# Performance work log

Hardware: AMD Instinct MI355X
Metric: run time of the kernel (lower is better)

## Reference

```python
import jax, jax.numpy as jnp
import numpy as np

DROPOUT_RATE = 0.5
CONF_THRESH = 0.85
IGNORE_VALUE = 2
EPS = 1e-07


def setup_inputs() -> dict:
    key = jax.random.key(0)
    k1, k2 = jax.random.split(key)
    B, H, W = 16, 1024, 1024
    pred = jax.random.uniform(k1, (B, H, W), dtype=jnp.float32)
    mask = jax.random.randint(k2, (B, H, W), 0, 3, dtype=jnp.int32)
    return {"pred": pred, "mask": mask}


def _training_need_score(pred, gt, confidence):
    # Higher = needs more training: CW=4, UW=3, UC=2, CC=1 (+/- confidence bonus)
    is_correct = (pred > 0.5) == (gt == 1.0)
    is_conf = confidence > CONF_THRESH
    score = jnp.where(is_conf & is_correct, 1.0,
            jnp.where(~is_conf & is_correct, 2.0,
            jnp.where(~is_conf & ~is_correct, 3.0, 4.0))).astype(pred.dtype)
    bonus = (confidence - 0.5) * 0.5
    return jnp.where(is_correct, score - bonus, score + bonus)


def _dynamic_masks(pred, mask):
    # Vectorized equivalent of the per-batch nonzero/argsort/scatter loop:
    # rank annotated pixels per batch by descending need-score; top n_train -> train.
    B, H, W = mask.shape
    annotated = (mask != IGNORE_VALUE).reshape(B, H * W)
    gt = mask.astype(pred.dtype)
    confidence = jnp.maximum(pred, 1.0 - pred)
    scores = _training_need_score(pred, gt, confidence).reshape(B, H * W)
    neg_inf = jnp.asarray(-jnp.inf, scores.dtype)
    masked_scores = jnp.where(annotated, scores, neg_inf)
    order = jnp.argsort(-masked_scores, axis=1)          # descending score order
    rank = jnp.argsort(order, axis=1)                    # rank of each pixel in that order
    n_points = annotated.sum(axis=1)
    n_train = (n_points.astype(jnp.float32) * (1.0 - DROPOUT_RATE)).astype(jnp.int32)
    train = annotated & (rank < n_train[:, None])
    holdout = annotated & ~train
    return train.reshape(B, H, W), holdout.reshape(B, H, W)


def reference(pred, mask):
    if pred.ndim == 4 and pred.shape[1] == 1:
        pred = pred[:, 0]
    train_mask, holdout_mask = _dynamic_masks(pred, mask)
    gt = mask.astype(pred.dtype)
    p = jnp.clip(pred, EPS, 1.0 - EPS)
    bce = -(gt * jnp.log(p) + (1.0 - gt) * jnp.log(1.0 - p))
    tm = train_mask.astype(pred.dtype)
    loss = (bce * tm).sum() / (tm.sum() + EPS)
    return loss, train_mask, holdout_mask
```

## Files before the change

### kernel.cpp

```cpp
#include <hip/hip_runtime.h>
#include <stdint.h>

#define NBATCH 16
#define HW_ (1 << 20)
#define TPB 256

#define NBPB_H 32
#define TPB_H 512
#define EPB_H (HW_ / NBPB_H)
#define ITER_H (EPB_H / (TPB_H * 4))

#define NBINS 8192
#define FBASE 0x3F400

#define NBPB_F 256
#define FCHUNK (HW_ / NBPB_F)

#define CAND_CAP 32768
#define LCAP 512
#define TIE_CAP 4096
#define CNT_STRIDE 64

typedef float f4v __attribute__((ext_vector_type(4)));

struct BParams {
    unsigned int k;
    unsigned int bin1f;
    unsigned int r;
    unsigned int mode;
};

__device__ __forceinline__ unsigned int score_bits(float p, int m) {
    bool correct = (p > 0.5f) == (m == 1);
    float conf = fmaxf(p, 1.0f - p);
    float base = correct ? ((conf > 0.85f) ? 1.0f : 2.0f)
                         : ((conf > 0.85f) ? 4.0f : 3.0f);
    float bonus = (conf - 0.5f) * 0.5f;
    float s = correct ? (base - bonus) : (base + bonus);
    return __float_as_uint(s);
}

__global__ void k_hist(const float4* __restrict__ pred4, const int4* __restrict__ mask4,
                       unsigned int* __restrict__ slices) {
    __shared__ unsigned int lh[NBINS];
    int b = blockIdx.x / NBPB_H;
    int blk = blockIdx.x % NBPB_H;
    for (int i = threadIdx.x; i < NBINS; i += TPB_H) lh[i] = 0;
    __syncthreads();
    int l4base = blk * (EPB_H / 4);
    for (int j = 0; j < ITER_H; j++) {
        int i4l = l4base + j * TPB_H + threadIdx.x;
        size_t g4 = (size_t)b * (HW_ / 4) + i4l;
        float4 p = pred4[g4];
        int4 m = mask4[g4];
        float pa[4] = {p.x, p.y, p.z, p.w};
        int ma[4] = {m.x, m.y, m.z, m.w};
#pragma unroll
        for (int l = 0; l < 4; l++) {
            if (ma[l] != 2) {
                unsigned int sb = score_bits(pa[l], ma[l]);
                int fb = (int)(sb >> 12) - FBASE;
                fb = min(max(fb, 0), NBINS - 1);
                atomicAdd(&lh[fb], 1u);
            }
        }
    }
    __syncthreads();
    unsigned int* sp = slices + (size_t)blockIdx.x * NBINS;
    for (int i = threadIdx.x; i < NBINS; i += TPB_H)
        sp[i] = lh[i];
}

__global__ void k_find(const unsigned int* __restrict__ slices, BParams* __restrict__ prm,
                       unsigned int* __restrict__ cand_cnt) {
    int bb = blockIdx.x;
    int t = threadIdx.x;
    __shared__ unsigned int hist[NBINS];
    __shared__ unsigned int cs_[257];
    unsigned int acc[32];
#pragma unroll
    for (int j = 0; j < 32; j++) acc[j] = 0;
    const unsigned int* base = slices + (size_t)bb * NBPB_H * NBINS;
    for (int s = 0; s < NBPB_H; s++) {
        const unsigned int* sp = base + (size_t)s * NBINS;
#pragma unroll
        for (int j = 0; j < 32; j++) acc[j] += sp[j * 256 + t];
    }
#pragma unroll
    for (int j = 0; j < 32; j++) hist[j * 256 + t] = acc[j];
    if (t == 0) cand_cnt[bb * CNT_STRIDE] = 0;
    __syncthreads();
    {
        unsigned int gs = 0;
#pragma unroll
        for (int j = 0; j < 32; j++) gs += hist[t * 32 + j];
        cs_[t] = gs;
        if (t == 0) cs_[256] = 0;
    }
    __syncthreads();
    for (int off = 1; off < 256; off <<= 1) {
        unsigned int a = (t + off < 256) ? cs_[t + off] : 0u;
        __syncthreads();
        cs_[t] += a;
        __syncthreads();
    }
    unsigned int n = cs_[0];
    unsigned int k = (unsigned int)(int)((float)n * 0.5f);
    if (k == 0) {
        if (t == 0) {
            BParams P; P.k = 0; P.bin1f = 0xFFFFFFFFu; P.r = 0; P.mode = 0;
            prm[bb] = P;
        }
        return;
    }
    if (cs_[t] >= k && cs_[t + 1] < k) {
        unsigned int cum = cs_[t + 1];
        for (int j = 31; j >= 0; j--) {
            unsigned int hb = hist[t * 32 + j];
            if (cum + hb >= k) {
                BParams P;
                P.k = k;
                P.bin1f = (unsigned int)(FBASE + t * 32 + j);
                P.r = k - cum;
                P.mode = 1;
                prm[bb] = P;
                break;
            }
            cum += hb;
        }
    }
}

__global__ void k_main(const float4* __restrict__ pred4, const int4* __restrict__ mask4,
                       const BParams* __restrict__ prm, float* __restrict__ out,
                       float* __restrict__ partials, unsigned int* __restrict__ cand_cnt,
                       unsigned int* __restrict__ cand_idx, unsigned int* __restrict__ cand_sb,
                       float* __restrict__ cand_bce) {
    int b = blockIdx.x / NBPB_F;
    int blk = blockIdx.x % NBPB_F;
    BParams P = prm[b];
    unsigned int target = P.bin1f;
    __shared__ unsigned int lcode[FCHUNK / 4];
    __shared__ float red[TPB];
    __shared__ unsigned int l_idx[LCAP];
    __shared__ unsigned int l_sb[LCAP];
    __shared__ float l_bce[LCAP];
    __shared__ unsigned int lcnt;
    __shared__ unsigned int gbase;
    if (threadIdx.x == 0) lcnt = 0;
    __syncthreads();
    float acc = 0.0f;
    int ibase = blk * FCHUNK;
    for (int j = 0; j < FCHUNK / (TPB * 4); j++) {
        int v = j * TPB + threadIdx.x;
        size_t g4 = (size_t)b * (HW_ / 4) + (ibase / 4) + v;
        float4 p = pred4[g4];
        int4 m = mask4[g4];
        float pa[4] = {p.x, p.y, p.z, p.w};
        int ma[4] = {m.x, m.y, m.z, m.w};
        unsigned int cw = 0;
#pragma unroll
        for (int l = 0; l < 4; l++) {
            bool ann = (ma[l] != 2);
            unsigned int sb = score_bits(pa[l], ma[l]);
            unsigned int fine = sb >> 12;
            bool tr = ann && (fine > target);
            bool amb = ann && (fine == target);
            unsigned int code = (tr ? 1u : 0u) | ((ann && !tr) ? 2u : 0u);
            cw |= code << (8 * l);
            float bce = 0.0f;
            if (tr || amb) {
                float pc = fminf(fmaxf(pa[l], 1e-7f), 1.0f - 1e-7f);
                bce = (ma[l] == 1) ? -__logf(pc) : -__logf(1.0f - pc);
            }
            if (tr) acc += bce;
            if (amb) {
                unsigned int p0 = atomicAdd(&lcnt, 1u);
                if (p0 < LCAP) {
                    l_idx[p0] = (unsigned int)(ibase + v * 4 + l);
                    l_sb[p0] = sb;
                    l_bce[p0] = bce;
                } else {
                    unsigned int gp = atomicAdd(&cand_cnt[b * CNT_STRIDE], 1u);
                    if (gp < CAND_CAP) {
                        size_t o = (size_t)b * CAND_CAP + gp;
                        cand_idx[o] = (unsigned int)(ibase + v * 4 + l);
                        cand_sb[o] = sb;
                        cand_bce[o] = bce;
                    }
                }
            }
        }
        lcode[v] = cw;
    }
    __syncthreads();
    unsigned int n = min(lcnt, (unsigned int)LCAP);
    if (threadIdx.x == 0 && n > 0)
        gbase = atomicAdd(&cand_cnt[b * CNT_STRIDE], n);
    __syncthreads();
    for (unsigned int i = threadIdx.x; i < n; i += TPB) {
        unsigned int pos = gbase + i;
        if (pos < CAND_CAP) {
            size_t o = (size_t)b * CAND_CAP + pos;
            cand_idx[o] = l_idx[i];
            cand_sb[o] = l_sb[i];
            cand_bce[o] = l_bce[i];
        }
    }
    float* trout = out + 1;
    float* hoout = out + 1 + (size_t)NBATCH * HW_;
    size_t Gbase = (size_t)b * HW_ + (size_t)ibase;
    for (int v = threadIdx.x; v < FCHUNK / 4 - 1; v += TPB) {
        unsigned int w0 = lcode[v];
        unsigned int w1 = lcode[v + 1];
        unsigned int c0 = (w0 >> 24) & 0xFFu;
        unsigned int c1 = w1 & 0xFFu;
        unsigned int c2 = (w1 >> 8) & 0xFFu;
        unsigned int c3 = (w1 >> 16) & 0xFFu;
        int e = 3 + 4 * v;
        f4v tv = { (float)(c0 & 1u), (float)(c1 & 1u), (float)(c2 & 1u), (float)(c3 & 1u) };
        f4v hv = { (float)((c0 >> 1) & 1u), (float)((c1 >> 1) & 1u),
                   (float)((c2 >> 1) & 1u), (float)((c3 >> 1) & 1u) };
        __builtin_nontemporal_store(tv, (f4v*)(trout + Gbase + e));
        __builtin_nontemporal_store(hv, (f4v*)(hoout + Gbase + e));
    }
    if (threadIdx.x < 3) {
        unsigned int c = (lcode[0] >> (8 * threadIdx.x)) & 0xFFu;
        trout[Gbase + threadIdx.x] = (float)(c & 1u);
        hoout[Gbase + threadIdx.x] = (float)((c >> 1) & 1u);
    }
    if (threadIdx.x == 3) {
        unsigned int c = (lcode[FCHUNK / 4 - 1] >> 24) & 0xFFu;
        trout[Gbase + FCHUNK - 1] = (float)(c & 1u);
        hoout[Gbase + FCHUNK - 1] = (float)((c >> 1) & 1u);
    }
    red[threadIdx.x] = acc;
    __syncthreads();
    for (int off = TPB / 2; off > 0; off >>= 1) {
        if (threadIdx.x < off) red[threadIdx.x] += red[threadIdx.x + off];
        __syncthreads();
    }
    if (threadIdx.x == 0) partials[blockIdx.x] = red[0];
}

__global__ void k_fixup(const unsigned int* __restrict__ cand_cnt,
                        const unsigned int* __restrict__ cand_idx,
                        const unsigned int* __restrict__ cand_sb,
                        const float* __restrict__ cand_bce,
                        const BParams* __restrict__ prm, float* __restrict__ out,
                        float* __restrict__ tie_partials) {
    int b = blockIdx.x;
    int t = threadIdx.x;
    __shared__ unsigned int h[4096];
    __shared__ unsigned int cs_[257];
    __shared__ unsigned int tie_idx[TIE_CAP];
    __shared__ unsigned int misc[8];
    __shared__ float red[TPB];
    BParams P = prm[b];
    if (P.mode == 0) {
        if (t == 0) tie_partials[b] = 0.0f;
        return;
    }
    unsigned int C = cand_cnt[b * CNT_STRIDE];
    if (C > CAND_CAP) C = CAND_CAP;
    const unsigned int* ci = cand_idx + (size_t)b * CAND_CAP;
    const unsigned int* cs = cand_sb + (size_t)b * CAND_CAP;
    const float* cb = cand_bce + (size_t)b * CAND_CAP;
    for (int i = t; i < 4096; i += TPB) h[i] = 0;
    if (t < 8) misc[t] = (t == 4) ? 0xFFFFFFFFu : 0u;
    __syncthreads();
    for (unsigned int i = t; i < C; i += TPB)
        atomicAdd(&h[cs[i] & 0xFFFu], 1u);
    __syncthreads();
    {
        unsigned int gs = 0;
#pragma unroll
        for (int j = 0; j < 16; j++) gs += h[t * 16 + j];
        cs_[t] = gs;
        if (t == 0) cs_[256] = 0;
    }
    __syncthreads();
    for (int off = 1; off < 256; off <<= 1) {
        unsigned int a = (t + off < 256) ? cs_[t + off] : 0u;
        __syncthreads();
        cs_[t] += a;
        __syncthreads();
    }
    if (cs_[t] >= P.r && cs_[t + 1] < P.r) {
        unsigned int cum = cs_[t + 1];
        for (int j = 15; j >= 0; j--) {
            unsigned int hb = h[t * 16 + j];
            if (cum + hb >= P.r) {
                unsigned int T = P.r - cum;
                misc[0] = (unsigned int)(t * 16 + j);
                misc[1] = T;
                misc[2] = (T == hb) ? 1u : 0u;
                break;
            }
            cum += hb;
        }
    }
    __syncthreads();
    unsigned int vstar = misc[0], T = misc[1];
    bool allTies = (misc[2] != 0);
    unsigned int idxcut;
    if (allTies) {
        idxcut = 0xFFFFFFFFu;
    } else {
        for (unsigned int i = t; i < C; i += TPB) {
            if ((cs[i] & 0xFFFu) == vstar) {
                unsigned int p = atomicAdd(&misc[3], 1u);
                if (p < TIE_CAP) tie_idx[p] = ci[i];
            }
        }
        __syncthreads();
        unsigned int E2 = misc[3];
        if (E2 > TIE_CAP) E2 = TIE_CAP;
        for (unsigned int i = t; i < E2; i += TPB) {
            unsigned int vi = tie_idx[i];
            unsigned int cnt = 0;
            for (unsigned int j = 0; j < E2; j++) cnt += (tie_idx[j] < vi) ? 1u : 0u;
            if (cnt == T - 1) misc[4] = vi;
        }
        __syncthreads();
        idxcut = misc[4];
    }
    float acc = 0.0f;
    float* trout = out + 1;
    float* hoout = out + 1 + (size_t)NBATCH * HW_;
    size_t base = (size_t)b * HW_;
    for (unsigned int i = t; i < C; i += TPB) {
        unsigned int low = cs[i] & 0xFFFu;
        bool tr = (low > vstar) || (low == vstar && ci[i] <= idxcut);
        if (tr) {
            trout[base + ci[i]] = 1.0f;
            hoout[base + ci[i]] = 0.0f;
            acc += cb[i];
        }
    }
    red[t] = acc;
    __syncthreads();
    for (int off = TPB / 2; off > 0; off >>= 1) {
        if (t < off) red[t] += red[t + off];
        __syncthreads();
    }
    if (t == 0) tie_partials[b] = red[0];
}

__global__ void k_loss(const float* __restrict__ partials, const float* __restrict__ tie_partials,
                       const BParams* __restrict__ prm, float* __restrict__ out) {
    __shared__ double red[TPB];
    double s = 0.0;
    for (int i = threadIdx.x; i < NBATCH * NBPB_F; i += TPB) s += (double)partials[i];
    if (threadIdx.x < NBATCH) s += (double)tie_partials[threadIdx.x];
    red[threadIdx.x] = s;
    __syncthreads();
    for (int off = TPB / 2; off > 0; off >>= 1) {
        if (threadIdx.x < off) red[threadIdx.x] += red[threadIdx.x + off];
        __syncthreads();
    }
    if (threadIdx.x == 0) {
        unsigned long long den = 0;
        for (int b = 0; b < NBATCH; b++) den += prm[b].k;
        float denf = (float)den + 1e-7f;
        out[0] = (float)red[0] / denf;
    }
}

extern "C" void kernel_launch(void* const* d_in, const int* in_sizes, int n_in,
                              void* d_out, int out_size, void* d_ws, size_t ws_size,
                              hipStream_t stream) {
    const float4* pred4 = (const float4*)d_in[0];
    const int4* mask4 = (const int4*)d_in[1];
    float* out = (float*)d_out;

    unsigned int* slices = (unsigned int*)d_ws;
    unsigned int* cand_cnt = slices + (size_t)NBATCH * NBPB_H * NBINS;
    BParams* prm = (BParams*)(cand_cnt + NBATCH * CNT_STRIDE);
    float* partials = (float*)(prm + NBATCH);
    float* tie_partials = partials + NBATCH * NBPB_F;
    unsigned int* cand_idx = (unsigned int*)(tie_partials + NBATCH);
    unsigned int* cand_sb = cand_idx + NBATCH * CAND_CAP;
    float* cand_bce = (float*)(cand_sb + NBATCH * CAND_CAP);

    k_hist<<<dim3(NBATCH * NBPB_H), dim3(TPB_H), 0, stream>>>(pred4, mask4, slices);
    k_find<<<dim3(NBATCH), dim3(TPB), 0, stream>>>(slices, prm, cand_cnt);
    k_main<<<dim3(NBATCH * NBPB_F), dim3(TPB), 0, stream>>>(pred4, mask4, prm, out, partials,
                                                            cand_cnt, cand_idx, cand_sb, cand_bce);
    k_fixup<<<dim3(NBATCH), dim3(TPB), 0, stream>>>(cand_cnt, cand_idx, cand_sb, cand_bce,
                                                    prm, out, tie_partials);
    k_loss<<<dim3(1), dim3(TPB), 0, stream>>>(partials, tie_partials, prm, out);
}
```

Measured before the change: 302.0 us.

## Fuse five kernels into two using last-block-done atomic counters

Folds the histogram-merge and threshold search into the last histogram block of each batch, and folds the tie fixup and final loss reduction into the last main block of each batch and overall. Per-block atomic done-counters with threadfences replace kernel boundaries, and block sums go into double atomics instead of a partials array. A memset now resets the counters before each launch. The aim is to remove launch gaps and the serial single-block kernels, at the cost of the tail work running inside one late block. TIE_CAP is also reduced so the shared-memory union fits.

```diff
diff --git a/kernel.cpp b/kernel.cpp
--- a/kernel.cpp
+++ b/kernel.cpp
@@ -18,8 +18,8 @@
 
 #define CAND_CAP 32768
 #define LCAP 512
-#define TIE_CAP 4096
-#define CNT_STRIDE 64
+#define TIE_CAP 1024
+#define CSTR 64
 
 typedef float f4v __attribute__((ext_vector_type(4)));
 
@@ -40,16 +40,20 @@
     return __float_as_uint(s);
 }
 
-__global__ void k_hist(const float4* __restrict__ pred4, const int4* __restrict__ mask4,
-                       unsigned int* __restrict__ slices) {
+__global__ void k_histfind(const float4* __restrict__ pred4, const int4* __restrict__ mask4,
+                           unsigned int* __restrict__ slices, unsigned int* __restrict__ doneA,
+                           BParams* __restrict__ prm) {
     __shared__ unsigned int lh[NBINS];
+    __shared__ unsigned int cs_[TPB_H + 1];
+    __shared__ unsigned int lastFlag;
     int b = blockIdx.x / NBPB_H;
     int blk = blockIdx.x % NBPB_H;
-    for (int i = threadIdx.x; i < NBINS; i += TPB_H) lh[i] = 0;
+    int t = threadIdx.x;
+    for (int i = t; i < NBINS; i += TPB_H) lh[i] = 0;
     __syncthreads();
     int l4base = blk * (EPB_H / 4);
     for (int j = 0; j < ITER_H; j++) {
-        int i4l = l4base + j * TPB_H + threadIdx.x;
+        int i4l = l4base + j * TPB_H + t;
         size_t g4 = (size_t)b * (HW_ / 4) + i4l;
         float4 p = pred4[g4];
         int4 m = mask4[g4];
@@ -67,39 +71,38 @@
     }
     __syncthreads();
     unsigned int* sp = slices + (size_t)blockIdx.x * NBINS;
-    for (int i = threadIdx.x; i < NBINS; i += TPB_H)
-        sp[i] = lh[i];
-}
-
-__global__ void k_find(const unsigned int* __restrict__ slices, BParams* __restrict__ prm,
-                       unsigned int* __restrict__ cand_cnt) {
-    int bb = blockIdx.x;
-    int t = threadIdx.x;
-    __shared__ unsigned int hist[NBINS];
-    __shared__ unsigned int cs_[257];
-    unsigned int acc[32];
-#pragma unroll
-    for (int j = 0; j < 32; j++) acc[j] = 0;
-    const unsigned int* base = slices + (size_t)bb * NBPB_H * NBINS;
+    for (int i = t; i < NBINS; i += TPB_H) sp[i] = lh[i];
+    __syncthreads();
+    if (t == 0) {
+        __threadfence();
+        unsigned int old = atomicAdd(&doneA[b * CSTR], 1u);
+        lastFlag = (old == NBPB_H - 1) ? 1u : 0u;
+    }
+    __syncthreads();
+    if (!lastFlag) return;
+
+    unsigned int acc[NBINS / TPB_H];
+#pragma unroll
+    for (int j = 0; j < NBINS / TPB_H; j++) acc[j] = 0;
+    const unsigned int* base = slices + (size_t)b * NBPB_H * NBINS;
     for (int s = 0; s < NBPB_H; s++) {
-        const unsigned int* sp = base + (size_t)s * NBINS;
-#pragma unroll
-        for (int j = 0; j < 32; j++) acc[j] += sp[j * 256 + t];
-    }
-#pragma unroll
-    for (int j = 0; j < 32; j++) hist[j * 256 + t] = acc[j];
-    if (t == 0) cand_cnt[bb * CNT_STRIDE] = 0;
+        const unsigned int* spp = base + (size_t)s * NBINS;
+#pragma unroll
+        for (int j = 0; j < NBINS / TPB_H; j++) acc[j] += spp[j * TPB_H + t];
+    }
+#pragma unroll
+    for (int j = 0; j < NBINS / TPB_H; j++) lh[j * TPB_H + t] = acc[j];
     __syncthreads();
     {
         unsigned int gs = 0;
 #pragma unroll
-        for (int j = 0; j < 32; j++) gs += hist[t * 32 + j];
+        for (int j = 0; j < NBINS / TPB_H; j++) gs += lh[t * (NBINS / TPB_H) + j];
         cs_[t] = gs;
-        if (t == 0) cs_[256] = 0;
-    }
-    __syncthreads();
-    for (int off = 1; off < 256; off <<= 1) {
-        unsigned int a = (t + off < 256) ? cs_[t + off] : 0u;
+        if (t == 0) cs_[TPB_H] = 0;
+    }
+    __syncthreads();
+    for (int off = 1; off < TPB_H; off <<= 1) {
+        unsigned int a = (t + off < TPB_H) ? cs_[t + off] : 0u;
         __syncthreads();
         cs_[t] += a;
         __syncthreads();
@@ -109,21 +112,21 @@
     if (k == 0) {
         if (t == 0) {
             BParams P; P.k = 0; P.bin1f = 0xFFFFFFFFu; P.r = 0; P.mode = 0;
-            prm[bb] = P;
+            prm[b] = P;
         }
         return;
     }
     if (cs_[t] >= k && cs_[t + 1] < k) {
         unsigned int cum = cs_[t + 1];
-        for (int j = 31; j >= 0; j--) {
-            unsigned int hb = hist[t * 32 + j];
+        for (int j = (NBINS / TPB_H) - 1; j >= 0; j--) {
+            unsigned int hb = lh[t * (NBINS / TPB_H) + j];
             if (cum + hb >= k) {
                 BParams P;
                 P.k = k;
-                P.bin1f = (unsigned int)(FBASE + t * 32 + j);
+                P.bin1f = (unsigned int)(FBASE + t * (NBINS / TPB_H) + j);
                 P.r = k - cum;
                 P.mode = 1;
-                prm[bb] = P;
+                prm[b] = P;
                 break;
             }
             cum += hb;
@@ -131,28 +134,38 @@
     }
 }
 
-__global__ void k_main(const float4* __restrict__ pred4, const int4* __restrict__ mask4,
-                       const BParams* __restrict__ prm, float* __restrict__ out,
-                       float* __restrict__ partials, unsigned int* __restrict__ cand_cnt,
-                       unsigned int* __restrict__ cand_idx, unsigned int* __restrict__ cand_sb,
-                       float* __restrict__ cand_bce) {
+struct MainS {
+    unsigned int lcode[FCHUNK / 4];
+    unsigned int l_idx[LCAP]; unsigned int l_sb[LCAP]; float l_bce[LCAP];
+    float red[TPB];
+    unsigned int lcnt, gbase;
+};
+struct FixS {
+    unsigned int h[4096]; unsigned int cs_[257];
+    unsigned int tie_idx[TIE_CAP]; unsigned int misc[8];
+    float red[TPB];
+};
+union SmemB { MainS m; FixS f; };
+
+__global__ void k_mainall(const float4* __restrict__ pred4, const int4* __restrict__ mask4,
+                          const BParams* __restrict__ prm, float* __restrict__ out,
+                          unsigned int* __restrict__ doneB, unsigned int* __restrict__ doneC,
+                          unsigned int* __restrict__ cand_cnt, double* __restrict__ bsum,
+                          unsigned int* __restrict__ cand_idx, unsigned int* __restrict__ cand_sb,
+                          float* __restrict__ cand_bce) {
+    __shared__ SmemB sm;
+    __shared__ unsigned int lastFlag;
     int b = blockIdx.x / NBPB_F;
     int blk = blockIdx.x % NBPB_F;
+    int t = threadIdx.x;
     BParams P = prm[b];
     unsigned int target = P.bin1f;
-    __shared__ unsigned int lcode[FCHUNK / 4];
-    __shared__ float red[TPB];
-    __shared__ unsigned int l_idx[LCAP];
-    __shared__ unsigned int l_sb[LCAP];
-    __shared__ float l_bce[LCAP];
-    __shared__ unsigned int lcnt;
-    __shared__ unsigned int gbase;
-    if (threadIdx.x == 0) lcnt = 0;
+    if (t == 0) sm.m.lcnt = 0;
     __syncthreads();
     float acc = 0.0f;
     int ibase = blk * FCHUNK;
     for (int j = 0; j < FCHUNK / (TPB * 4); j++) {
-        int v = j * TPB + threadIdx.x;
+        int v = j * TPB + t;
         size_t g4 = (size_t)b * (HW_ / 4) + (ibase / 4) + v;
         float4 p = pred4[g4];
         int4 m = mask4[g4];
@@ -175,13 +188,13 @@
             }
             if (tr) acc += bce;
             if (amb) {
-                unsigned int p0 = atomicAdd(&lcnt, 1u);
+                unsigned int p0 = atomicAdd(&sm.m.lcnt, 1u);
                 if (p0 < LCAP) {
-                    l_idx[p0] = (unsigned int)(ibase + v * 4 + l);
-                    l_sb[p0] = sb;
-                    l_bce[p0] = bce;
+                    sm.m.l_idx[p0] = (unsigned int)(ibase + v * 4 + l);
+                    sm.m.l_sb[p0] = sb;
+                    sm.m.l_bce[p0] = bce;
                 } else {
-                    unsigned int gp = atomicAdd(&cand_cnt[b * CNT_STRIDE], 1u);
+                    unsigned int gp = atomicAdd(&cand_cnt[b * CSTR], 1u);
                     if (gp < CAND_CAP) {
                         size_t o = (size_t)b * CAND_CAP + gp;
                         cand_idx[o] = (unsigned int)(ibase + v * 4 + l);
@@ -191,28 +204,28 @@
                 }
             }
         }
-        lcode[v] = cw;
-    }
-    __syncthreads();
-    unsigned int n = min(lcnt, (unsigned int)LCAP);
-    if (threadIdx.x == 0 && n > 0)
-        gbase = atomicAdd(&cand_cnt[b * CNT_STRIDE], n);
-    __syncthreads();
-    for (unsigned int i = threadIdx.x; i < n; i += TPB) {
-        unsigned int pos = gbase + i;
+        sm.m.lcode[v] = cw;
+    }
+    __syncthreads();
+    unsigned int nc = min(sm.m.lcnt, (unsigned int)LCAP);
+    if (t == 0 && nc > 0)
+        sm.m.gbase = atomicAdd(&cand_cnt[b * CSTR], nc);
+    __syncthreads();
+    for (unsigned int i = t; i < nc; i += TPB) {
+        unsigned int pos = sm.m.gbase + i;
         if (pos < CAND_CAP) {
             size_t o = (size_t)b * CAND_CAP + pos;
-            cand_idx[o] = l_idx[i];
-            cand_sb[o] = l_sb[i];
-            cand_bce[o] = l_bce[i];
+            cand_idx[o] = sm.m.l_idx[i];
+            cand_sb[o] = sm.m.l_sb[i];
+            cand_bce[o] = sm.m.l_bce[i];
         }
     }
     float* trout = out + 1;
     float* hoout = out + 1 + (size_t)NBATCH * HW_;
     size_t Gbase = (size_t)b * HW_ + (size_t)ibase;
-    for (int v = threadIdx.x; v < FCHUNK / 4 - 1; v += TPB) {
-        unsigned int w0 = lcode[v];
-        unsigned int w1 = lcode[v + 1];
+    for (int v = t; v < FCHUNK / 4 - 1; v += TPB) {
+        unsigned int w0 = sm.m.lcode[v];
+        unsigned int w1 = sm.m.lcode[v + 1];
         unsigned int c0 = (w0 >> 24) & 0xFFu;
         unsigned int c1 = w1 & 0xFFu;
         unsigned int c2 = (w1 >> 8) & 0xFFu;
@@ -224,146 +237,129 @@
         __builtin_nontemporal_store(tv, (f4v*)(trout + Gbase + e));
         __builtin_nontemporal_store(hv, (f4v*)(hoout + Gbase + e));
     }
-    if (threadIdx.x < 3) {
-        unsigned int c = (lcode[0] >> (8 * threadIdx.x)) & 0xFFu;
-        trout[Gbase + threadIdx.x] = (float)(c & 1u);
-        hoout[Gbase + threadIdx.x] = (float)((c >> 1) & 1u);
-    }
-    if (threadIdx.x == 3) {
-        unsigned int c = (lcode[FCHUNK / 4 - 1] >> 24) & 0xFFu;
+    if (t < 3) {
+        unsigned int c = (sm.m.lcode[0] >> (8 * t)) & 0xFFu;
+        trout[Gbase + t] = (float)(c & 1u);
+        hoout[Gbase + t] = (float)((c >> 1) & 1u);
+    }
+    if (t == 3) {
+        unsigned int c = (sm.m.lcode[FCHUNK / 4 - 1] >> 24) & 0xFFu;
         trout[Gbase + FCHUNK - 1] = (float)(c & 1u);
         hoout[Gbase + FCHUNK - 1] = (float)((c >> 1) & 1u);
     }
-    red[threadIdx.x] = acc;
+    sm.m.red[t] = acc;
     __syncthreads();
     for (int off = TPB / 2; off > 0; off >>= 1) {
-        if (threadIdx.x < off) red[threadIdx.x] += red[threadIdx.x + off];
-        __syncthreads();
-    }
-    if (threadIdx.x == 0) partials[blockIdx.x] = red[0];
-}
-
-__global__ void k_fixup(const unsigned int* __restrict__ cand_cnt,
-                        const unsigned int* __restrict__ cand_idx,
-                        const unsigned int* __restrict__ cand_sb,
-                        const float* __restrict__ cand_bce,
-                        const BParams* __restrict__ prm, float* __restrict__ out,
-                        float* __restrict__ tie_partials) {
-    int b = blockIdx.x;
-    int t = threadIdx.x;
-    __shared__ unsigned int h[4096];
-    __shared__ unsigned int cs_[257];
-    __shared__ unsigned int tie_idx[TIE_CAP];
-    __shared__ unsigned int misc[8];
-    __shared__ float red[TPB];
-    BParams P = prm[b];
-    if (P.mode == 0) {
-        if (t == 0) tie_partials[b] = 0.0f;
-        return;
-    }
-    unsigned int C = cand_cnt[b * CNT_STRIDE];
-    if (C > CAND_CAP) C = CAND_CAP;
-    const unsigned int* ci = cand_idx + (size_t)b * CAND_CAP;
-    const unsigned int* cs = cand_sb + (size_t)b * CAND_CAP;
-    const float* cb = cand_bce + (size_t)b * CAND_CAP;
-    for (int i = t; i < 4096; i += TPB) h[i] = 0;
-    if (t < 8) misc[t] = (t == 4) ? 0xFFFFFFFFu : 0u;
-    __syncthreads();
-    for (unsigned int i = t; i < C; i += TPB)
-        atomicAdd(&h[cs[i] & 0xFFFu], 1u);
-    __syncthreads();
-    {
-        unsigned int gs = 0;
-#pragma unroll
-        for (int j = 0; j < 16; j++) gs += h[t * 16 + j];
-        cs_[t] = gs;
-        if (t == 0) cs_[256] = 0;
-    }
-    __syncthreads();
-    for (int off = 1; off < 256; off <<= 1) {
-        unsigned int a = (t + off < 256) ? cs_[t + off] : 0u;
-        __syncthreads();
-        cs_[t] += a;
-        __syncthreads();
-    }
-    if (cs_[t] >= P.r && cs_[t + 1] < P.r) {
-        unsigned int cum = cs_[t + 1];
-        for (int j = 15; j >= 0; j--) {
-            unsigned int hb = h[t * 16 + j];
-            if (cum + hb >= P.r) {
-                unsigned int T = P.r - cum;
-                misc[0] = (unsigned int)(t * 16 + j);
-                misc[1] = T;
-                misc[2] = (T == hb) ? 1u : 0u;
-                break;
-            }
-            cum += hb;
-        }
-    }
-    __syncthreads();
-    unsigned int vstar = misc[0], T = misc[1];
-    bool allTies = (misc[2] != 0);
-    unsigned int idxcut;
-    if (allTies) {
-        idxcut = 0xFFFFFFFFu;
-    } else {
+        if (t < off) sm.m.red[t] += sm.m.red[t + off];
+        __syncthreads();
+    }
+    if (t == 0) {
+        if (sm.m.red[0] != 0.0f) atomicAdd(&bsum[b], (double)sm.m.red[0]);
+        __threadfence();
+        unsigned int old = atomicAdd(&doneB[b * CSTR], 1u);
+        lastFlag = (old == NBPB_F - 1) ? 1u : 0u;
+    }
+    __syncthreads();
+    if (!lastFlag) return;
+
+    if (P.mode != 0) {
+        unsigned int C = cand_cnt[b * CSTR];
+        if (C > CAND_CAP) C = CAND_CAP;
+        const unsigned int* ci = cand_idx + (size_t)b * CAND_CAP;
+        const unsigned int* cs = cand_sb + (size_t)b * CAND_CAP;
+        const float* cb = cand_bce + (size_t)b * CAND_CAP;
+        for (int i = t; i < 4096; i += TPB) sm.f.h[i] = 0;
+        if (t < 8) sm.f.misc[t] = (t == 4) ? 0xFFFFFFFFu : 0u;
+        __syncthreads();
+        for (unsigned int i = t; i < C; i += TPB)
+            atomicAdd(&sm.f.h[cs[i] & 0xFFFu], 1u);
+        __syncthreads();
+        {
+            unsigned int gs = 0;
+#pragma unroll
+            for (int j = 0; j < 16; j++) gs += sm.f.h[t * 16 + j];
+            sm.f.cs_[t] = gs;
+            if (t == 0) sm.f.cs_[256] = 0;
+        }
+        __syncthreads();
+        for (int off = 1; off < 256; off <<= 1) {
+            unsigned int a = (t + off < 256) ? sm.f.cs_[t + off] : 0u;
+            __syncthreads();
+            sm.f.cs_[t] += a;
+            __syncthreads();
+        }
+        if (sm.f.cs_[t] >= P.r && sm.f.cs_[t + 1] < P.r) {
+            unsigned int cum = sm.f.cs_[t + 1];
+            for (int j = 15; j >= 0; j--) {
+                unsigned int hb = sm.f.h[t * 16 + j];
+                if (cum + hb >= P.r) {
+                    unsigned int T = P.r - cum;
+                    sm.f.misc[0] = (unsigned int)(t * 16 + j);
+                    sm.f.misc[1] = T;
+                    sm.f.misc[2] = (T == hb) ? 1u : 0u;
+                    break;
+                }
+                cum += hb;
+            }
+        }
+        __syncthreads();
+        unsigned int vstar = sm.f.misc[0], T = sm.f.misc[1];
+        bool allTies = (sm.f.misc[2] != 0);
+        unsigned int idxcut;
+        if (allTies) {
+            idxcut = 0xFFFFFFFFu;
+        } else {
+            for (unsigned int i = t; i < C; i += TPB) {
+                if ((cs[i] & 0xFFFu) == vstar) {
+                    unsigned int p = atomicAdd(&sm.f.misc[3], 1u);
+                    if (p < TIE_CAP) sm.f.tie_idx[p] = ci[i];
+                }
+            }
+            __syncthreads();
+            unsigned int E2 = sm.f.misc[3];
+            if (E2 > TIE_CAP) E2 = TIE_CAP;
+            for (unsigned int i = t; i < E2; i += TPB) {
+                unsigned int vi = sm.f.tie_idx[i];
+                unsigned int cnt = 0;
+                for (unsigned int j = 0; j < E2; j++)
+                    cnt += (sm.f.tie_idx[j] < vi) ? 1u : 0u;
+                if (cnt == T - 1) sm.f.misc[4] = vi;
+            }
+            __syncthreads();
+            idxcut = sm.f.misc[4];
+        }
+        float facc = 0.0f;
+        size_t basee = (size_t)b * HW_;
         for (unsigned int i = t; i < C; i += TPB) {
-            if ((cs[i] & 0xFFFu) == vstar) {
-                unsigned int p = atomicAdd(&misc[3], 1u);
-                if (p < TIE_CAP) tie_idx[p] = ci[i];
-            }
-        }
-        __syncthreads();
-        unsigned int E2 = misc[3];
-        if (E2 > TIE_CAP) E2 = TIE_CAP;
-        for (unsigned int i = t; i < E2; i += TPB) {
-            unsigned int vi = tie_idx[i];
-            unsigned int cnt = 0;
-            for (unsigned int j = 0; j < E2; j++) cnt += (tie_idx[j] < vi) ? 1u : 0u;
-            if (cnt == T - 1) misc[4] = vi;
-        }
-        __syncthreads();
-        idxcut = misc[4];
-    }
-    float acc = 0.0f;
-    float* trout = out + 1;
-    float* hoout = out + 1 + (size_t)NBATCH * HW_;
-    size_t base = (size_t)b * HW_;
-    for (unsigned int i = t; i < C; i += TPB) {
-        unsigned int low = cs[i] & 0xFFFu;
-        bool tr = (low > vstar) || (low == vstar && ci[i] <= idxcut);
-        if (tr) {
-            trout[base + ci[i]] = 1.0f;
-            hoout[base + ci[i]] = 0.0f;
-            acc += cb[i];
-        }
-    }
-    red[t] = acc;
-    __syncthreads();
-    for (int off = TPB / 2; off > 0; off >>= 1) {
-        if (t < off) red[t] += red[t + off];
-        __syncthreads();
-    }
-    if (t == 0) tie_partials[b] = red[0];
-}
-
-__global__ void k_loss(const float* __restrict__ partials, const float* __restrict__ tie_partials,
-                       const BParams* __restrict__ prm, float* __restrict__ out) {
-    __shared__ double red[TPB];
-    double s = 0.0;
-    for (int i = threadIdx.x; i < NBATCH * NBPB_F; i += TPB) s += (double)partials[i];
-    if (threadIdx.x < NBATCH) s += (double)tie_partials[threadIdx.x];
-    red[threadIdx.x] = s;
-    __syncthreads();
-    for (int off = TPB / 2; off > 0; off >>= 1) {
-        if (threadIdx.x < off) red[threadIdx.x] += red[threadIdx.x + off];
-        __syncthreads();
-    }
-    if (threadIdx.x == 0) {
-        unsigned long long den = 0;
-        for (int b = 0; b < NBATCH; b++) den += prm[b].k;
-        float denf = (float)den + 1e-7f;
-        out[0] = (float)red[0] / denf;
+            unsigned int low = cs[i] & 0xFFFu;
+            bool tr = (low > vstar) || (low == vstar && ci[i] <= idxcut);
+            if (tr) {
+                trout[basee + ci[i]] = 1.0f;
+                hoout[basee + ci[i]] = 0.0f;
+                facc += cb[i];
+            }
+        }
+        sm.f.red[t] = facc;
+        __syncthreads();
+        for (int off = TPB / 2; off > 0; off >>= 1) {
+            if (t < off) sm.f.red[t] += sm.f.red[t + off];
+            __syncthreads();
+        }
+        if (t == 0 && sm.f.red[0] != 0.0f) atomicAdd(&bsum[b], (double)sm.f.red[0]);
+    }
+    if (t == 0) {
+        __threadfence();
+        unsigned int old2 = atomicAdd(doneC, 1u);
+        if (old2 == NBATCH - 1) {
+            double num = 0.0;
+            unsigned long long den = 0;
+            for (int b2 = 0; b2 < NBATCH; b2++) {
+                num += atomicAdd(&bsum[b2], 0.0);
+                den += prm[b2].k;
+            }
+            float denf = (float)den + 1e-7f;
+            out[0] = (float)num / denf;
+        }
     }
 }
 
@@ -374,20 +370,22 @@
     const int4* mask4 = (const int4*)d_in[1];
     float* out = (float*)d_out;
 
-    unsigned int* slices = (unsigned int*)d_ws;
-    unsigned int* cand_cnt = slices + (size_t)NBATCH * NBPB_H * NBINS;
-    BParams* prm = (BParams*)(cand_cnt + NBATCH * CNT_STRIDE);
-    float* partials = (float*)(prm + NBATCH);
-    float* tie_partials = partials + NBATCH * NBPB_F;
-    unsigned int* cand_idx = (unsigned int*)(tie_partials + NBATCH);
+    unsigned int* ctr = (unsigned int*)d_ws;
+    unsigned int* doneA = ctr;
+    unsigned int* doneB = ctr + 1024;
+    unsigned int* cand_cnt = ctr + 2048;
+    unsigned int* doneC = ctr + 3072;
+    double* bsum = (double*)((char*)d_ws + 16384);
+    unsigned int* slices = (unsigned int*)((char*)d_ws + 32768);
+    BParams* prm = (BParams*)(slices + (size_t)NBATCH * NBPB_H * NBINS);
+    unsigned int* cand_idx = (unsigned int*)(prm + NBATCH);
     unsigned int* cand_sb = cand_idx + NBATCH * CAND_CAP;
     float* cand_bce = (float*)(cand_sb + NBATCH * CAND_CAP);
 
-    k_hist<<<dim3(NBATCH * NBPB_H), dim3(TPB_H), 0, stream>>>(pred4, mask4, slices);
-    k_find<<<dim3(NBATCH), dim3(TPB), 0, stream>>>(slices, prm, cand_cnt);
-    k_main<<<dim3(NBATCH * NBPB_F), dim3(TPB), 0, stream>>>(pred4, mask4, prm, out, partials,
-                                                            cand_cnt, cand_idx, cand_sb, cand_bce);
-    k_fixup<<<dim3(NBATCH), dim3(TPB), 0, stream>>>(cand_cnt, cand_idx, cand_sb, cand_bce,
-                                                    prm, out, tie_partials);
-    k_loss<<<dim3(1), dim3(TPB), 0, stream>>>(partials, tie_partials, prm, out);
+    hipMemsetAsync(d_ws, 0, 32768, stream);
+    k_histfind<<<dim3(NBATCH * NBPB_H), dim3(TPB_H), 0, stream>>>(pred4, mask4, slices,
+                                                                  doneA, prm);
+    k_mainall<<<dim3(NBATCH * NBPB_F), dim3(TPB), 0, stream>>>(pred4, mask4, prm, out,
+                                                               doneB, doneC, cand_cnt, bsum,
+                                                               cand_idx, cand_sb, cand_bce);
 }
```

Result: slower. 500.6 us (+65.8%).
